# Performance work log

Hardware: AMD Instinct MI355X
Metric: run time of the kernel (lower is better)

The kernel has to match this reference:

```python
import jax, jax.numpy as jnp
import numpy as np

N = 100000   # num nodes
E = 3200000  # num edges (avg degree 32)
H = 64       # hidden_dim
EPS = 1e-5   # batchnorm eps


def setup_inputs() -> dict:
    key = jax.random.key(0)
    ks = jax.random.split(key, 12)
    def gl(k, shp):  # glorot-ish init
        fan = shp[0]
        return jax.random.normal(k, shp, dtype=jnp.float32) / np.sqrt(fan)
    return dict(
        x=jax.random.normal(ks[0], (N, 4), dtype=jnp.float32),
        src=jax.random.randint(ks[1], (E,), 0, N, dtype=jnp.int32),
        dst=jax.random.randint(ks[2], (E,), 0, N, dtype=jnp.int32),
        W0=gl(ks[3], (4, H)), b0=jnp.zeros((H,), jnp.float32),
        W1=gl(ks[4], (H, H)), b1=jnp.zeros((H,), jnp.float32),
        g0=jnp.ones((H,), jnp.float32), be0=jnp.zeros((H,), jnp.float32),
        g1=jnp.ones((H,), jnp.float32), be1=jnp.zeros((H,), jnp.float32),
        Wm0=gl(ks[5], (H, H)), bm0=jnp.zeros((H,), jnp.float32),
        Wm1=gl(ks[6], (H, H // 2)), bm1=jnp.zeros((H // 2,), jnp.float32),
        Wm2=gl(ks[7], (H // 2, 1)), bm2=jnp.zeros((1,), jnp.float32),
    )


def gcn_conv(x, W, b, src, dst, n):
    # PyG GCNConv: add self-loops, symmetric D^-1/2 (A+I) D^-1/2 normalization,
    # linear transform, scatter-add aggregation at destination, then bias.
    h = x @ W                                   # [n, out]
    loop = jnp.arange(n, dtype=src.dtype)
    s = jnp.concatenate([src, loop])            # sources incl self-loops
    d = jnp.concatenate([dst, loop])            # targets incl self-loops
    deg = jax.ops.segment_sum(jnp.ones_like(d, dtype=h.dtype), d, num_segments=n)
    dinv = jnp.where(deg > 0, jax.lax.rsqrt(deg), 0.0)
    norm = dinv[s] * dinv[d]                    # [E+n]
    msg = h[s] * norm[:, None]                  # gather + scale
    out = jax.ops.segment_sum(msg, d, num_segments=n)  # scatter-add
    return out + b


def batchnorm(x, g, b):
    # training-mode BatchNorm1d over the node dimension (biased variance)
    mu = jnp.mean(x, axis=0)
    var = jnp.mean(jnp.square(x - mu), axis=0)
    return g * (x - mu) * jax.lax.rsqrt(var + EPS) + b


def reference(x, src, dst, W0, b0, W1, b1, g0, be0, g1, be1,
              Wm0, bm0, Wm1, bm1, Wm2, bm2):
    n = x.shape[0]
    h = gcn_conv(x, W0, b0, src, dst, n)
    h = jax.nn.relu(batchnorm(h, g0, be0))      # dropout = identity (eval)
    h = gcn_conv(h, W1, b1, src, dst, n)
    h = jax.nn.relu(batchnorm(h, g1, be1))
    h = jax.nn.relu(h @ Wm0 + bm0)
    h = jax.nn.relu(h @ Wm1 + bm1)
    return jax.nn.sigmoid(h @ Wm2 + bm2)        # [n, 1] collision probs
```

## Files before the change

### kernel.cpp

```cpp
#include <hip/hip_runtime.h>
#include <hip/hip_fp16.h>
#include <math.h>

#define HD 64
#define EPS 1e-5f
#define BSH 8
#define BSZ 256
#define T1 4096
#define BCAP 10240

__device__ __forceinline__ float atomAddF(float* p, float v) {
    return unsafeAtomicAdd(p, v);
}


__global__ __launch_bounds__(512) void k_ginit(int* __restrict__ gcur) {
    int t = threadIdx.x;
    gcur[t] = t * BCAP;
}

__global__ __launch_bounds__(256) void k_bucket(const int* __restrict__ src,
        const int* __restrict__ dst, int* __restrict__ gcur,
        unsigned* __restrict__ bedges, int e, int nbuck) {
    __shared__ int hist[512];
    __shared__ int base[512];
    int t = threadIdx.x;
    int tile = blockIdx.x * T1;
    int lim = min(e - tile, T1);
    hist[t] = 0; hist[t + 256] = 0;
    __syncthreads();
    int d_[16], s_[16];
    bool full = (lim == T1);
    if (full) {
        const int4* d4 = (const int4*)(dst + tile);
        const int4* s4 = (const int4*)(src + tile);
        #pragma unroll
        for (int j = 0; j < 4; ++j) {
            int4 dv = d4[j * 256 + t];
            int4 sv = s4[j * 256 + t];
            d_[4 * j + 0] = dv.x; d_[4 * j + 1] = dv.y;
            d_[4 * j + 2] = dv.z; d_[4 * j + 3] = dv.w;
            s_[4 * j + 0] = sv.x; s_[4 * j + 1] = sv.y;
            s_[4 * j + 2] = sv.z; s_[4 * j + 3] = sv.w;
        }
        #pragma unroll
        for (int j = 0; j < 16; ++j) atomicAdd(&hist[d_[j] >> BSH], 1);
    } else {
        for (int j = t; j < lim; j += 256)
            atomicAdd(&hist[dst[tile + j] >> BSH], 1);
    }
    __syncthreads();
    for (int b = t; b < nbuck; b += 256) {
        int h = hist[b];
        base[b] = (h > 0) ? atomicAdd(&gcur[b], h) : 0;
        hist[b] = 0;
    }
    __syncthreads();
    if (full) {
        #pragma unroll
        for (int j = 0; j < 16; ++j) {
            int bk = d_[j] >> BSH;
            int loc = atomicAdd(&hist[bk], 1);
            bedges[base[bk] + loc] =
                ((unsigned)(d_[j] & (BSZ - 1)) << 17) | (unsigned)s_[j];
        }
    } else {
        for (int j = t; j < lim; j += 256) {
            int d = dst[tile + j], s = src[tile + j];
            int bk = d >> BSH;
            int loc = atomicAdd(&hist[bk], 1);
            bedges[base[bk] + loc] = ((unsigned)(d & (BSZ - 1)) << 17) | (unsigned)s;
        }
    }
}

__global__ __launch_bounds__(512) void k_bscan(const int* __restrict__ gcur,
        int* __restrict__ boff, int* __restrict__ row_ptr, int nb, int n, int e) {
    __shared__ int sc[512];
    int t = threadIdx.x;
    int v = (t < nb) ? (gcur[t] - t * BCAP) : 0;
    sc[t] = v;
    __syncthreads();
    int acc = v;
    for (int off = 1; off < 512; off <<= 1) {
        int x = (t >= off) ? sc[t - off] : 0;
        __syncthreads();
        acc += x;
        sc[t] = acc;
        __syncthreads();
    }
    boff[t] = acc - v;
    if (t == 0) row_ptr[n] = e;
}

__global__ __launch_bounds__(256) void k_build(const unsigned* __restrict__ bedges,
        const int* __restrict__ boff, int* __restrict__ row_ptr,
        unsigned* __restrict__ csr, float* __restrict__ dinv, int n) {
    __shared__ int hist[BSZ];
    __shared__ int cur[BSZ];
    __shared__ int sc[256];
    int b = blockIdx.x, t = threadIdx.x;
    int nodebase = b << BSH;
    int cbase = boff[b];
    int cnt = boff[b + 1] - cbase;
    const unsigned* bed = bedges + (size_t)b * BCAP;
    hist[t] = 0;
    __syncthreads();
    int cnt4 = cnt & ~3;
    for (int jj = t * 4; jj < cnt4; jj += 1024) {
        uint4 p = *(const uint4*)(bed + jj);
        atomicAdd(&hist[p.x >> 17], 1); atomicAdd(&hist[p.y >> 17], 1);
        atomicAdd(&hist[p.z >> 17], 1); atomicAdd(&hist[p.w >> 17], 1);
    }
    for (int jj = cnt4 + t; jj < cnt; jj += 256)
        atomicAdd(&hist[bed[jj] >> 17], 1);
    __syncthreads();
    int a = hist[t];
    sc[t] = a;
    __syncthreads();
    int acc = a;
    for (int off = 1; off < 256; off <<= 1) {
        int x = (t >= off) ? sc[t - off] : 0;
        __syncthreads();
        acc += x;
        sc[t] = acc;
        __syncthreads();
    }
    int e0 = cbase + acc - a;
    cur[t] = e0;
    int node = nodebase + t;
    if (node < n) { row_ptr[node] = e0; dinv[node] = rsqrtf((float)(a + 1)); }
    __syncthreads();
    for (int jj = t * 4; jj < cnt4; jj += 1024) {
        uint4 p = *(const uint4*)(bed + jj);
        int p0 = atomicAdd(&cur[p.x >> 17], 1); csr[p0] = p.x;
        int p1 = atomicAdd(&cur[p.y >> 17], 1); csr[p1] = p.y;
        int p2 = atomicAdd(&cur[p.z >> 17], 1); csr[p2] = p.z;
        int p3 = atomicAdd(&cur[p.w >> 17], 1); csr[p3] = p.w;
    }
    for (int jj = cnt4 + t; jj < cnt; jj += 256) {
        unsigned p = bed[jj];
        int pos = atomicAdd(&cur[p >> 17], 1);
        csr[pos] = p;
    }
}


__global__ __launch_bounds__(256) void k_lin0(const float* __restrict__ x,
        const float* __restrict__ W0, const float* __restrict__ dinv,
        __half* __restrict__ A, int n_nodes) {
    __shared__ float w[4 * HD];
    int t = threadIdx.x;
    w[t] = W0[t];
    __syncthreads();
    int n = blockIdx.x * 4 + (t >> 6);
    int c = t & 63;
    if (n >= n_nodes) return;
    float x0 = x[n * 4 + 0], x1 = x[n * 4 + 1], x2 = x[n * 4 + 2], x3 = x[n * 4 + 3];
    float v = x0 * w[c] + x1 * w[64 + c] + x2 * w[128 + c] + x3 * w[192 + c];
    A[((size_t)n << 6) + c] = __float2half(v * dinv[n]);
}

__global__ __launch_bounds__(256) void k_aggr(const int* __restrict__ row_ptr,
        const unsigned* __restrict__ pedges, const __half* __restrict__ A,
        const float* __restrict__ dinv, const float* __restrict__ bias,
        float* __restrict__ B, float* __restrict__ stats, int n_nodes) {
    __shared__ float acc[64 * 65];
    __shared__ float ls[4][64], ls2[4][64];
    int t = threadIdx.x;
    for (int i = t; i < 64 * 65; i += 256) acc[i] = 0.f;
    int nodebase = blockIdx.x << 6;
    int nend = min(nodebase + 64, n_nodes);
    int ebeg = row_ptr[nodebase];
    int eend = row_ptr[nend];
    int nedges = eend - ebeg;
    __syncthreads();

    int wv = t >> 6, lane = t & 63;
    int sub = lane >> 4, ch = lane & 15;
    int s = wv * 4 + sub;
    int sbeg = ebeg + (int)(((long long)nedges * s) >> 4);
    int send = ebeg + (int)(((long long)nedges * (s + 1)) >> 4);
    const uint2* A2 = (const uint2*)A;

    float a0 = 0.f, a1 = 0.f, a2 = 0.f, a3 = 0.f;
    int cur = -1;

    #define FLUSH() if (cur >= 0) {                                            \
        int o_ = cur * 65 + (ch << 2);                                         \
        atomicAdd(&acc[o_ + 0], a0); atomicAdd(&acc[o_ + 1], a1);              \
        atomicAdd(&acc[o_ + 2], a2); atomicAdd(&acc[o_ + 3], a3); }

    #define PROC(P, U) {                                                       \
        int d_ = (int)((P) >> 17) & 63;                                        \
        if (d_ != cur) { FLUSH(); a0 = a1 = a2 = a3 = 0.f; cur = d_; }         \
        float2 f01_ = __half22float2(*(const __half2*)&(U).x);                 \
        float2 f23_ = __half22float2(*(const __half2*)&(U).y);                 \
        a0 += f01_.x; a1 += f01_.y; a2 += f23_.x; a3 += f23_.y; }

    int j = sbeg;
    for (; j + 16 <= send; j += 16) {
        unsigned p[16];
        uint2 u[16];
        #pragma unroll
        for (int k = 0; k < 16; ++k) p[k] = pedges[j + k];
        #pragma unroll
        for (int k = 0; k < 16; ++k)
            u[k] = A2[(((size_t)(p[k] & 0x1FFFFu)) << 4) + ch];
        #pragma unroll
        for (int k = 0; k < 16; ++k) PROC(p[k], u[k]);
    }
    for (; j < send; ++j) {
        unsigned p0 = pedges[j];
        uint2 u0 = A2[(((size_t)(p0 & 0x1FFFFu)) << 4) + ch];
        PROC(p0, u0);
    }
    FLUSH();
    #undef PROC
    #undef FLUSH
    __syncthreads();

    int c = lane;
    float st = 0.f, st2 = 0.f;
    for (int r = wv; r < 64; r += 4) {
        int node = nodebase + r;
        if (node < n_nodes) {
            float v = acc[r * 65 + c] + __half2float(A[((size_t)node << 6) + c]);
            v = dinv[node] * v + bias[c];
            B[((size_t)node << 6) + c] = v;
            st += v; st2 += v * v;
        }
    }
    ls[wv][c] = st; ls2[wv][c] = st2;
    __syncthreads();
    if (t < 64) {
        atomAddF(&stats[t], ls[0][t] + ls[1][t] + ls[2][t] + ls[3][t]);
        atomAddF(&stats[64 + t], ls2[0][t] + ls2[1][t] + ls2[2][t] + ls2[3][t]);
    }
}

__global__ __launch_bounds__(256) void k_lin1(const float* __restrict__ B,
        const float* __restrict__ W, const float* __restrict__ dinv,
        const float* __restrict__ stats, const float* __restrict__ g,
        const float* __restrict__ be, __half* __restrict__ A, int n_nodes) {
    __shared__ float w[HD * HD];
    __shared__ float rows[16][65];
    __shared__ float scb[64], shb[64];
    int t = threadIdx.x;
    for (int i = t; i < HD * HD; i += 256) w[i] = W[i];
    if (t < 64) {
        float inv_n = 1.0f / (float)n_nodes;
        float mu = stats[t] * inv_n;
        float var = stats[64 + t] * inv_n - mu * mu;
        float sc = g[t] * rsqrtf(var + EPS);
        scb[t] = sc;
        shb[t] = be[t] - mu * sc;
    }
    int wv = t >> 6, lane = t & 63;
    int nsub = lane >> 4, quad = lane & 15;
    const float4* w4 = (const float4*)w;
    int ngroups = (n_nodes + 15) >> 4;
    for (int gidx = blockIdx.x; gidx < ngroups; gidx += gridDim.x) {
        __syncthreads();
        int nb0 = gidx << 4;
        #pragma unroll
        for (int i = 0; i < 4; ++i) {
            int idx = t + (i << 8);
            int r = idx >> 6, c = idx & 63;
            int nn = nb0 + r;
            float v = (nn < n_nodes) ? B[((size_t)nn << 6) + c] : 0.f;
            rows[r][c] = fmaxf(scb[c] * v + shb[c], 0.f);
        }
        __syncthreads();
        int r = (wv << 2) + nsub;
        int node = nb0 + r;
        if (node < n_nodes) {
            float a0 = 0.f, a1 = 0.f, a2 = 0.f, a3 = 0.f;
            #pragma unroll 8
            for (int k = 0; k < 64; ++k) {
                float hv = rows[r][k];
                float4 wq = w4[(k << 4) + quad];
                a0 = fmaf(hv, wq.x, a0); a1 = fmaf(hv, wq.y, a1);
                a2 = fmaf(hv, wq.z, a2); a3 = fmaf(hv, wq.w, a3);
            }
            float dv = dinv[node];
            __half2 h01 = __floats2half2_rn(a0 * dv, a1 * dv);
            __half2 h23 = __floats2half2_rn(a2 * dv, a3 * dv);
            uint2 uu;
            uu.x = *(unsigned*)&h01;
            uu.y = *(unsigned*)&h23;
            *(uint2*)(A + ((size_t)node << 6) + (quad << 2)) = uu;
        }
    }
}

__global__ __launch_bounds__(256) void k_mlp(const float* __restrict__ B,
        const float* __restrict__ stats, const float* __restrict__ g,
        const float* __restrict__ be,
        const float* __restrict__ Wm0, const float* __restrict__ bm0,
        const float* __restrict__ Wm1, const float* __restrict__ bm1,
        const float* __restrict__ Wm2, const float* __restrict__ bm2,
        float* __restrict__ out, int n_nodes) {
    __shared__ float rows[32][66];
    __shared__ float scb[64], shb[64];
    int t = threadIdx.x;
    if (t < 64) {
        float inv_n = 1.0f / (float)n_nodes;
        float mu = stats[t] * inv_n;
        float var = stats[64 + t] * inv_n - mu * mu;
        float sc = g[t] * rsqrtf(var + EPS);
        scb[t] = sc;
        shb[t] = be[t] - mu * sc;
    }
    __syncthreads();
    int nbase = blockIdx.x * 32;
    #pragma unroll 8
    for (int i = 0; i < 8; ++i) {
        int idx = t + i * 256;
        int r = idx >> 6, c = idx & 63;
        int nn = nbase + r;
        float v = (nn < n_nodes) ? B[((size_t)nn << 6) + c] : 0.f;
        rows[r][c] = fmaxf(scb[c] * v + shb[c], 0.f);
    }
    __syncthreads();

    int w = t >> 6, j = t & 63;
    int rb = w * 8;
    float acc0[8];
    float b0j = bm0[j];
    #pragma unroll
    for (int i = 0; i < 8; ++i) acc0[i] = b0j;
    #pragma unroll 4
    for (int k = 0; k < 64; k += 2) {
        float wv0 = Wm0[k * 64 + j];
        float wv1 = Wm0[(k + 1) * 64 + j];
        #pragma unroll
        for (int i = 0; i < 8; ++i) {
            float2 hv = *(const float2*)&rows[rb + i][k];
            acc0[i] = fmaf(hv.x, wv0, acc0[i]);
            acc0[i] = fmaf(hv.y, wv1, acc0[i]);
        }
    }
    #pragma unroll
    for (int i = 0; i < 8; ++i) rows[rb + i][j] = fmaxf(acc0[i], 0.f);
    __syncthreads();
    int h = j >> 5, ch2 = j & 31;
    int rb1 = rb + h * 4;
    float acc2[4];
    float b1j = bm1[ch2];
    #pragma unroll
    for (int i = 0; i < 4; ++i) acc2[i] = b1j;
    #pragma unroll 4
    for (int k = 0; k < 64; k += 2) {
        float wv0 = Wm1[k * 32 + ch2];
        float wv1 = Wm1[(k + 1) * 32 + ch2];
        #pragma unroll
        for (int i = 0; i < 4; ++i) {
            float2 hv = *(const float2*)&rows[rb1 + i][k];
            acc2[i] = fmaf(hv.x, wv0, acc2[i]);
            acc2[i] = fmaf(hv.y, wv1, acc2[i]);
        }
    }
    float wm2 = Wm2[ch2];
    float z[4];
    #pragma unroll
    for (int i = 0; i < 4; ++i) z[i] = fmaxf(acc2[i], 0.f) * wm2;
    #pragma unroll
    for (int d = 1; d < 32; d <<= 1) {
        #pragma unroll
        for (int i = 0; i < 4; ++i) z[i] += __shfl_xor(z[i], d, 64);
    }
    if (ch2 == 0) {
        float bb = bm2[0];
        #pragma unroll
        for (int i = 0; i < 4; ++i) {
            int nn = nbase + rb1 + i;
            if (nn < n_nodes)
                out[nn] = 1.0f / (1.0f + __expf(-(z[i] + bb)));
        }
    }
}

extern "C" void kernel_launch(void* const* d_in, const int* in_sizes, int n_in,
                              void* d_out, int out_size, void* d_ws, size_t ws_size,
                              hipStream_t stream) {
    const float* x   = (const float*)d_in[0];
    const int*   src = (const int*)d_in[1];
    const int*   dst = (const int*)d_in[2];
    const float* W0  = (const float*)d_in[3];
    const float* b0  = (const float*)d_in[4];
    const float* W1  = (const float*)d_in[5];
    const float* b1  = (const float*)d_in[6];
    const float* g0  = (const float*)d_in[7];
    const float* be0 = (const float*)d_in[8];
    const float* g1  = (const float*)d_in[9];
    const float* be1 = (const float*)d_in[10];
    const float* Wm0 = (const float*)d_in[11];
    const float* bm0 = (const float*)d_in[12];
    const float* Wm1 = (const float*)d_in[13];
    const float* bm1 = (const float*)d_in[14];
    const float* Wm2 = (const float*)d_in[15];
    const float* bm2 = (const float*)d_in[16];

    int n = in_sizes[0] / 4;
    int e = in_sizes[1];
    float* out = (float*)d_out;

    int nb = (n + BSZ - 1) >> BSH;

    char* ws = (char*)d_ws;
    auto alignup = [](size_t v) { return (v + 255) & ~(size_t)255; };
    size_t o = 0;
    int*      boff    = (int*)(ws + o);      o += alignup(513 * 4);
    int*      gcur    = (int*)(ws + o);      o += alignup(512 * 4);
    float*    stats   = (float*)(ws + o);    o += alignup(256 * 4);
    int*      row_ptr = (int*)(ws + o);      o += alignup((size_t)(n + 1) * 4);
    float*    dinv    = (float*)(ws + o);    o += alignup((size_t)n * 4);
    unsigned* bedges  = (unsigned*)(ws + o); o += alignup((size_t)nb * BCAP * 4);
    unsigned* csr     = (unsigned*)(ws + o); o += alignup((size_t)e * 4);
    __half*   A       = (__half*)(ws + o);   o += alignup((size_t)n * 64 * 2);
    float*    B       = (float*)(ws + o);

    int gN4    = (n + 3) / 4;
    int ntiles = (e + T1 - 1) / T1;
    int gMLP   = (n + 31) / 32;
    int gAGG   = (n + 63) / 64;

    (void)hipMemsetAsync(stats, 0, 256 * 4, stream);

    k_ginit<<<1, 512, 0, stream>>>(gcur);
    k_bucket<<<ntiles, 256, 0, stream>>>(src, dst, gcur, bedges, e, nb);
    k_bscan<<<1, 512, 0, stream>>>(gcur, boff, row_ptr, nb, n, e);
    k_build<<<nb, 256, 0, stream>>>(bedges, boff, row_ptr, csr, dinv, n);

    k_lin0<<<gN4, 256, 0, stream>>>(x, W0, dinv, A, n);
    k_aggr<<<gAGG, 256, 0, stream>>>(row_ptr, csr, A, dinv, b0, B, stats, n);

    k_lin1<<<2048, 256, 0, stream>>>(B, W1, dinv, stats, g0, be0, A, n);
    k_aggr<<<gAGG, 256, 0, stream>>>(row_ptr, csr, A, dinv, b1, B, stats + 128, n);

    k_mlp<<<gMLP, 256, 0, stream>>>(B, stats + 128, g1, be1,
                                    Wm0, bm0, Wm1, bm1, Wm2, bm2, out, n);
}
```

Before: 326.9 us.

## Fuse bucket scan and first linear layer into CSR build kernel

```diff
diff --git a/kernel.cpp b/kernel.cpp
--- a/kernel.cpp
+++ b/kernel.cpp
@@ -13,11 +13,6 @@
     return unsafeAtomicAdd(p, v);
 }
 
-
-__global__ __launch_bounds__(512) void k_ginit(int* __restrict__ gcur) {
-    int t = threadIdx.x;
-    gcur[t] = t * BCAP;
-}
 
 __global__ __launch_bounds__(256) void k_bucket(const int* __restrict__ src,
         const int* __restrict__ dst, int* __restrict__ gcur,
@@ -52,7 +47,7 @@
     __syncthreads();
     for (int b = t; b < nbuck; b += 256) {
         int h = hist[b];
-        base[b] = (h > 0) ? atomicAdd(&gcur[b], h) : 0;
+        base[b] = (h > 0) ? (b * BCAP + atomicAdd(&gcur[b], h)) : 0;
         hist[b] = 0;
     }
     __syncthreads();
@@ -74,36 +69,42 @@
     }
 }
 
-__global__ __launch_bounds__(512) void k_bscan(const int* __restrict__ gcur,
-        int* __restrict__ boff, int* __restrict__ row_ptr, int nb, int n, int e) {
-    __shared__ int sc[512];
-    int t = threadIdx.x;
-    int v = (t < nb) ? (gcur[t] - t * BCAP) : 0;
-    sc[t] = v;
-    __syncthreads();
-    int acc = v;
-    for (int off = 1; off < 512; off <<= 1) {
-        int x = (t >= off) ? sc[t - off] : 0;
-        __syncthreads();
-        acc += x;
-        sc[t] = acc;
-        __syncthreads();
-    }
-    boff[t] = acc - v;
-    if (t == 0) row_ptr[n] = e;
-}
-
 __global__ __launch_bounds__(256) void k_build(const unsigned* __restrict__ bedges,
-        const int* __restrict__ boff, int* __restrict__ row_ptr,
-        unsigned* __restrict__ csr, float* __restrict__ dinv, int n) {
+        const int* __restrict__ gcur, int* __restrict__ row_ptr,
+        unsigned* __restrict__ csr, float* __restrict__ dinv,
+        const float* __restrict__ x, const float* __restrict__ W0,
+        __half* __restrict__ A, int n, int nb, int e) {
     __shared__ int hist[BSZ];
     __shared__ int cur[BSZ];
     __shared__ int sc[256];
+    __shared__ int boffL[512];
+    __shared__ float w0s[256];
+    __shared__ float dinvs[BSZ];
     int b = blockIdx.x, t = threadIdx.x;
     int nodebase = b << BSH;
-    int cbase = boff[b];
-    int cnt = boff[b + 1] - cbase;
+
+    int c0 = (2 * t < nb) ? gcur[2 * t] : 0;
+    int c1 = (2 * t + 1 < nb) ? gcur[2 * t + 1] : 0;
+    int ps = c0 + c1;
+    sc[t] = ps;
+    w0s[t] = W0[t];
+    __syncthreads();
+    int acc = ps;
+    for (int off = 1; off < 256; off <<= 1) {
+        int xv = (t >= off) ? sc[t - off] : 0;
+        __syncthreads();
+        acc += xv;
+        sc[t] = acc;
+        __syncthreads();
+    }
+    boffL[2 * t] = acc - ps;
+    boffL[2 * t + 1] = acc - ps + c0;
+    if (t == 0 && b == 0) row_ptr[n] = e;
+    __syncthreads();
+    int cbase = boffL[b];
+    int cnt = (b < nb) ? gcur[b] : 0;
     const unsigned* bed = bedges + (size_t)b * BCAP;
+
     hist[t] = 0;
     __syncthreads();
     int cnt4 = cnt & ~3;
@@ -118,19 +119,22 @@
     int a = hist[t];
     sc[t] = a;
     __syncthreads();
-    int acc = a;
+    int acc2 = a;
     for (int off = 1; off < 256; off <<= 1) {
-        int x = (t >= off) ? sc[t - off] : 0;
-        __syncthreads();
-        acc += x;
-        sc[t] = acc;
-        __syncthreads();
-    }
-    int e0 = cbase + acc - a;
+        int xv = (t >= off) ? sc[t - off] : 0;
+        __syncthreads();
+        acc2 += xv;
+        sc[t] = acc2;
+        __syncthreads();
+    }
+    int e0 = cbase + acc2 - a;
     cur[t] = e0;
+    float dv = rsqrtf((float)(a + 1));
+    dinvs[t] = dv;
     int node = nodebase + t;
-    if (node < n) { row_ptr[node] = e0; dinv[node] = rsqrtf((float)(a + 1)); }
-    __syncthreads();
+    if (node < n) { row_ptr[node] = e0; dinv[node] = dv; }
+    __syncthreads();
+
     for (int jj = t * 4; jj < cnt4; jj += 1024) {
         uint4 p = *(const uint4*)(bed + jj);
         int p0 = atomicAdd(&cur[p.x >> 17], 1); csr[p0] = p.x;
@@ -143,23 +147,19 @@
         int pos = atomicAdd(&cur[p >> 17], 1);
         csr[pos] = p;
     }
-}
-
-
-__global__ __launch_bounds__(256) void k_lin0(const float* __restrict__ x,
-        const float* __restrict__ W0, const float* __restrict__ dinv,
-        __half* __restrict__ A, int n_nodes) {
-    __shared__ float w[4 * HD];
-    int t = threadIdx.x;
-    w[t] = W0[t];
-    __syncthreads();
-    int n = blockIdx.x * 4 + (t >> 6);
-    int c = t & 63;
-    if (n >= n_nodes) return;
-    float x0 = x[n * 4 + 0], x1 = x[n * 4 + 1], x2 = x[n * 4 + 2], x3 = x[n * 4 + 3];
-    float v = x0 * w[c] + x1 * w[64 + c] + x2 * w[128 + c] + x3 * w[192 + c];
-    A[((size_t)n << 6) + c] = __float2half(v * dinv[n]);
-}
+    __syncthreads();
+
+    int wv = t >> 6, c = t & 63;
+    for (int r = wv; r < BSZ; r += 4) {
+        int nd = nodebase + r;
+        if (nd >= n) continue;
+        float4 xv = *(const float4*)(x + nd * 4);
+        float v = xv.x * w0s[c] + xv.y * w0s[64 + c]
+                + xv.z * w0s[128 + c] + xv.w * w0s[192 + c];
+        A[((size_t)nd << 6) + c] = __float2half(v * dinvs[r]);
+    }
+}
+
 
 __global__ __launch_bounds__(256) void k_aggr(const int* __restrict__ row_ptr,
         const unsigned* __restrict__ pedges, const __half* __restrict__ A,
@@ -411,7 +411,6 @@
     char* ws = (char*)d_ws;
     auto alignup = [](size_t v) { return (v + 255) & ~(size_t)255; };
     size_t o = 0;
-    int*      boff    = (int*)(ws + o);      o += alignup(513 * 4);
     int*      gcur    = (int*)(ws + o);      o += alignup(512 * 4);
     float*    stats   = (float*)(ws + o);    o += alignup(256 * 4);
     int*      row_ptr = (int*)(ws + o);      o += alignup((size_t)(n + 1) * 4);
@@ -421,19 +420,16 @@
     __half*   A       = (__half*)(ws + o);   o += alignup((size_t)n * 64 * 2);
     float*    B       = (float*)(ws + o);
 
-    int gN4    = (n + 3) / 4;
     int ntiles = (e + T1 - 1) / T1;
     int gMLP   = (n + 31) / 32;
     int gAGG   = (n + 63) / 64;
 
-    (void)hipMemsetAsync(stats, 0, 256 * 4, stream);
-
-    k_ginit<<<1, 512, 0, stream>>>(gcur);
+    (void)hipMemsetAsync(gcur, 0, (512 + 256) * 4, stream);
+
     k_bucket<<<ntiles, 256, 0, stream>>>(src, dst, gcur, bedges, e, nb);
-    k_bscan<<<1, 512, 0, stream>>>(gcur, boff, row_ptr, nb, n, e);
-    k_build<<<nb, 256, 0, stream>>>(bedges, boff, row_ptr, csr, dinv, n);
-
-    k_lin0<<<gN4, 256, 0, stream>>>(x, W0, dinv, A, n);
+    k_build<<<nb, 256, 0, stream>>>(bedges, gcur, row_ptr, csr, dinv,
+                                    x, W0, A, n, nb, e);
+
     k_aggr<<<gAGG, 256, 0, stream>>>(row_ptr, csr, A, dinv, b0, B, stats, n);
 
     k_lin1<<<2048, 256, 0, stream>>>(B, W1, dinv, stats, g0, be0, A, n);
```

After: 325.8 us. No clear change (-0.3%).
